# Performance work log

Hardware: AMD Instinct MI355X
Metric: run time of the kernel (lower is better)

Reference implementation:

```python
import jax, jax.numpy as jnp
import numpy as np


def setup_inputs() -> dict:
    key = jax.random.key(0)
    k1, k2 = jax.random.split(key)
    latents = jax.random.normal(k1, (32, 1024, 64), dtype=jnp.float32)
    codebook = jax.random.normal(k2, (8192, 64), dtype=jnp.float32)
    return {"latents": latents, "codebook": codebook}


def reference(latents, codebook):
    # Faithful to: cdist(latents_flat, codebook) -> argmin(dim=1) -> reshape(B, L)
    B, L, D = latents.shape
    x = latents.reshape(-1, D)                         # (N, D)
    x2 = jnp.sum(x * x, axis=1, keepdims=True)         # (N, 1)
    c2 = jnp.sum(codebook * codebook, axis=1)          # (K,)
    # (N, K) distance matrix, then argmin reduction
    d2 = x2 - 2.0 * (x @ codebook.T) + c2[None, :]
    indices = jnp.argmin(d2, axis=1)                   # (N,)
    return indices.reshape(B, L)
```

## Files before the change

### kernel.cpp

```cpp
#include <hip/hip_runtime.h>
#include <stdint.h>


#define N_TOTAL 32768
#define K_CODES 8192
#define EPS_GAP 0.008f

typedef __attribute__((ext_vector_type(4)))  float  floatx4;
typedef __attribute__((ext_vector_type(8)))  __bf16 bf16x8;

#define O_C2    0u
#define O_CBSW  32768u
#define O_PS1   2129920u
#define O_PS2   2654208u
#define O_PI1   3178496u
#define O_CNT   3702784u
#define O_LIST  3703040u
#define O_SLOT  3834112u
#define WS_NEED 4096256u

__device__ __forceinline__ unsigned int fkey(float s) {
    unsigned int u = __float_as_uint(s);
    return (u & 0x80000000u) ? ~u : (u | 0x80000000u);
}

__device__ __forceinline__ void load_lds16(const void* g, void* l) {
    __builtin_amdgcn_global_load_lds(
        (const __attribute__((address_space(1))) unsigned int*)g,
        (__attribute__((address_space(3))) unsigned int*)l, 16, 0, 0);
}

__global__ __launch_bounds__(256) void vq_prep(
    const float4* __restrict__ cb, uint4* __restrict__ cbSw,
    float* __restrict__ c2, int* __restrict__ cnt) {
    __shared__ float red[256];
    const int m = threadIdx.x & 31, g = threadIdx.x >> 5;
    const int rb = blockIdx.x;
    if (rb == 0 && threadIdx.x == 0) *cnt = 0;
    float4 a = cb[(size_t)(rb * 32 + m) * 16 + g * 2];
    float4 b = cb[(size_t)(rb * 32 + m) * 16 + g * 2 + 1];
    float x[8] = {a.x, a.y, a.z, a.w, b.x, b.y, b.z, b.w};
    bf16x8 hv, lv;
    float ss = 0.f;
#pragma unroll
    for (int i = 0; i < 8; ++i) {
        float v  = x[i];
        __bf16 hb = (__bf16)v;
        float r  = v - (float)hb;
        hv[i] = hb;
        lv[i] = (__bf16)r;
        ss += v * v;
    }
    cbSw[(size_t)rb * 512 + g * 32 + m]       = __builtin_bit_cast(uint4, hv);
    cbSw[(size_t)rb * 512 + (8 + g) * 32 + m] = __builtin_bit_cast(uint4, lv);
    red[threadIdx.x] = ss;
    __syncthreads();
    if (threadIdx.x < 32) {
        float s = 0.f;
#pragma unroll
        for (int gg = 0; gg < 8; ++gg) s += red[threadIdx.x + 32 * gg];
        c2[rb * 32 + threadIdx.x] = s;
    }
}

__global__ __launch_bounds__(256, 4) void vq_mfma(
    const float4* __restrict__ lat, const uint4* __restrict__ cbSw,
    const float* __restrict__ c2,
    float* __restrict__ pS1, float* __restrict__ pS2, int* __restrict__ pI1) {
    __shared__ uint4 Bs[2][1024];
    const int tid = threadIdx.x;
    const int wr = tid >> 6, lane = tid & 63;
    const int c16 = lane & 15, h4 = lane >> 4;

    const int q = blockIdx.x * 64 + wr * 16 + c16;
    bf16x8 aH[2], aL[2];
#pragma unroll
    for (int c = 0; c < 2; ++c) {
        float4 v0 = lat[(size_t)q * 16 + c * 8 + h4 * 2];
        float4 v1 = lat[(size_t)q * 16 + c * 8 + h4 * 2 + 1];
        float x[8] = {v0.x, v0.y, v0.z, v0.w, v1.x, v1.y, v1.z, v1.w};
#pragma unroll
        for (int j = 0; j < 8; ++j) {
            float v  = x[j];
            __bf16 hb = (__bf16)v;
            aH[c][j] = hb;
            aL[c][j] = (__bf16)(v - (float)hb);
        }
    }

    float t1[4], t2[4]; int i1[4];
#pragma unroll
    for (int r = 0; r < 4; ++r) { t1[r] = -3e38f; t2[r] = -3e38f; i1[r] = 0; }

    const int kBase = blockIdx.y * 2048;
    const uint4* srcBase = cbSw + ((size_t)(kBase >> 5) << 9);
    const float* c2g = c2 + kBase + c16;

    float ccCur[4], ccNxt[4];
#pragma unroll
    for (int T = 0; T < 4; ++T) ccCur[T] = c2g[T * 16];
#pragma unroll
    for (int i = 0; i < 4; ++i)
        load_lds16(&srcBase[wr * 256 + i * 64 + lane], &Bs[0][wr * 256 + i * 64]);
    __syncthreads();

    int cur = 0;
    for (int stage = 0; stage < 32; ++stage) {
        if (stage + 1 < 32) {
            const uint4* sp = srcBase + (size_t)(stage + 1) * 1024;
#pragma unroll
            for (int i = 0; i < 4; ++i)
                load_lds16(&sp[wr * 256 + i * 64 + lane],
                           &Bs[cur ^ 1][wr * 256 + i * 64]);
#pragma unroll
            for (int T = 0; T < 4; ++T)
                ccNxt[T] = c2g[(stage + 1) * 64 + T * 16];
        }

        const int colBase = kBase + stage * 64 + c16;

        __builtin_amdgcn_s_setprio(1);
#pragma unroll
        for (int T = 0; T < 4; ++T) {
            const float nn = -0.5f * ccCur[T];
            const int col = colBase + T * 16;
            const int bb = (T >> 1) * 512 + (T & 1) * 16 + c16 + h4 * 32;
            bf16x8 bH0 = __builtin_bit_cast(bf16x8, Bs[cur][bb]);
            bf16x8 bH1 = __builtin_bit_cast(bf16x8, Bs[cur][bb + 128]);
            bf16x8 bL0 = __builtin_bit_cast(bf16x8, Bs[cur][bb + 256]);
            bf16x8 bL1 = __builtin_bit_cast(bf16x8, Bs[cur][bb + 384]);
            floatx4 acc = {nn, nn, nn, nn};
            acc = __builtin_amdgcn_mfma_f32_16x16x32_bf16(aH[0], bH0, acc, 0, 0, 0);
            acc = __builtin_amdgcn_mfma_f32_16x16x32_bf16(aH[1], bH1, acc, 0, 0, 0);
            acc = __builtin_amdgcn_mfma_f32_16x16x32_bf16(aL[0], bH0, acc, 0, 0, 0);
            acc = __builtin_amdgcn_mfma_f32_16x16x32_bf16(aL[1], bH1, acc, 0, 0, 0);
            acc = __builtin_amdgcn_mfma_f32_16x16x32_bf16(aH[0], bL0, acc, 0, 0, 0);
            acc = __builtin_amdgcn_mfma_f32_16x16x32_bf16(aH[1], bL1, acc, 0, 0, 0);
#pragma unroll
            for (int r = 0; r < 4; ++r) {
                float a = acc[r];
                bool gt = a > t1[r];
                t2[r] = __builtin_amdgcn_fmed3f(a, t1[r], t2[r]);
                t1[r] = fmaxf(t1[r], a);
                i1[r] = gt ? col : i1[r];
            }
        }
        __builtin_amdgcn_s_setprio(0);

        __syncthreads();
#pragma unroll
        for (int T = 0; T < 4; ++T) ccCur[T] = ccNxt[T];
        cur ^= 1;
    }

#pragma unroll
    for (int mask = 1; mask <= 8; mask <<= 1) {
#pragma unroll
        for (int r = 0; r < 4; ++r) {
            float o1 = __shfl_xor(t1[r], mask);
            float o2 = __shfl_xor(t2[r], mask);
            int   oi = __shfl_xor(i1[r], mask);
            float n2 = fmaxf(fmaxf(t2[r], o2), fminf(t1[r], o1));
            bool take = (o1 > t1[r]) || (o1 == t1[r] && oi < i1[r]);
            t1[r] = take ? o1 : t1[r];
            i1[r] = take ? oi : i1[r];
            t2[r] = n2;
        }
    }

    if (c16 == 0) {
        const int o0 = blockIdx.y * N_TOTAL;
        const int qb = blockIdx.x * 64 + wr * 16 + h4 * 4;
#pragma unroll
        for (int r = 0; r < 4; ++r) {
            pS1[o0 + qb + r] = -2.f * t1[r];
            pS2[o0 + qb + r] = -2.f * t2[r];
            pI1[o0 + qb + r] = i1[r];
        }
    }
}

__global__ void vq_merge4(const float* __restrict__ pS1, const float* __restrict__ pS2,
                          const int* __restrict__ pI1, int* __restrict__ out,
                          int* __restrict__ cnt, int* __restrict__ list,
                          unsigned long long* __restrict__ slot) {
    int q = blockIdx.x * 256 + threadIdx.x;
    float g1 = 3e38f, g2 = 3e38f;
    int   gi = 0x7FFFFFFF;
#pragma unroll
    for (int p = 0; p < 4; ++p) {
        float s1p = pS1[p * N_TOTAL + q];
        float s2p = pS2[p * N_TOTAL + q];
        int   i1p = pI1[p * N_TOTAL + q];
        bool take = (s1p < g1) || (s1p == g1 && i1p < gi);
        g2 = fminf(g2, fminf(s2p, take ? g1 : s1p));
        if (take) { g1 = s1p; gi = i1p; }
    }
    out[q] = gi;
    if (g2 - g1 < EPS_GAP) {
        int e = atomicAdd(cnt, 1);
        list[e] = q;
        slot[e] = 0xFFFFFFFFFFFFFFFFull;
    }
}

__global__ __launch_bounds__(256) void vq_exact2(
    const float4* __restrict__ lat, const float4* __restrict__ cb,
    const float* __restrict__ c2, const int* __restrict__ cnt,
    const int* __restrict__ list, unsigned long long* __restrict__ slot) {
    __shared__ float qv[4][64];
    const int n = *cnt;
    const int totalChunks = n * 8;
    const int wInB = threadIdx.x >> 6;
    const int lane = threadIdx.x & 63;

    for (int base = blockIdx.x * 4; base < totalChunks; base += gridDim.x * 4) {
        const int c = base + wInB;
        const bool act = c < totalChunks;
        int e = 0, q = 0, kb = 0;
        if (act) { e = c >> 3; q = list[e]; kb = (c & 7) << 10; }
        __syncthreads();
        if (act && lane < 16) {
            float4 v = lat[(size_t)q * 16 + lane];
            *(float4*)&qv[wInB][lane * 4] = v;
        }
        __syncthreads();
        if (act) {
            float best = 3e38f; int bi = 0;
#pragma unroll 2
            for (int i = 0; i < 16; ++i) {
                const int k = kb + i * 64 + lane;
                float dot = 0.f;
#pragma unroll
                for (int d4 = 0; d4 < 16; ++d4) {
                    float4 cv = cb[(size_t)k * 16 + d4];
                    dot += qv[wInB][d4 * 4 + 0] * cv.x + qv[wInB][d4 * 4 + 1] * cv.y
                         + qv[wInB][d4 * 4 + 2] * cv.z + qv[wInB][d4 * 4 + 3] * cv.w;
                }
                float s = c2[k] - 2.f * dot;
                if (s < best) { best = s; bi = k; }
            }
            unsigned long long p = ((unsigned long long)fkey(best) << 32) | (unsigned)bi;
#pragma unroll
            for (int mask = 1; mask <= 32; mask <<= 1) {
                unsigned long long o = __shfl_xor(p, mask);
                p = o < p ? o : p;
            }
            if (lane == 0) atomicMin(&slot[e], p);
        }
    }
}

__global__ void vq_write(const int* __restrict__ cnt, const int* __restrict__ list,
                         const unsigned long long* __restrict__ slot,
                         int* __restrict__ out) {
    int t = blockIdx.x * 256 + threadIdx.x;
    if (t < *cnt) out[list[t]] = (int)(slot[t] & 0xFFFFFFFFull);
}

#define BM 128
#define BN 128
#define PAD 68

__global__ void vq_norms_fb(const float4* __restrict__ cb, float* __restrict__ c2) {
    int t = blockIdx.x * 256 + threadIdx.x;
    int r = t >> 2, p = t & 3;
    float s = 0.f;
#pragma unroll
    for (int i = 0; i < 4; ++i) {
        float4 v = cb[r * 16 + p * 4 + i];
        s += v.x * v.x + v.y * v.y + v.z * v.z + v.w * v.w;
    }
    s += __shfl_xor(s, 1);
    s += __shfl_xor(s, 2);
    if (p == 0) c2[r] = s;
}

__global__ __launch_bounds__(256) void vq_fp32(
    const float4* __restrict__ lat, const float4* __restrict__ cb,
    const float* __restrict__ c2, int ktPer,
    int* __restrict__ outIdx, float* __restrict__ partS, int* __restrict__ partI,
    int writePartial) {
    __shared__ float As[BM][PAD];
    __shared__ float Bsf[BN][PAD];
    __shared__ float c2s[BN];
    const int tid = threadIdx.x;
    const int tx = tid & 15;
    const int ty = tid >> 4;
    const int nBase = blockIdx.x * BM;
    const int kt0 = blockIdx.y * ktPer;
    const int ktN = kt0 + ktPer;
#pragma unroll
    for (int r = 0; r < 8; ++r) {
        int f = tid + 256 * r;
        int mm = f >> 4, d4 = f & 15;
        float4 v = lat[(size_t)(nBase + mm) * 16 + d4];
        *(float4*)&As[mm][d4 * 4] = v;
    }
    float best[8]; int bidx[8];
#pragma unroll
    for (int ii = 0; ii < 8; ++ii) { best[ii] = 3e38f; bidx[ii] = 0; }
    for (int kt = kt0; kt < ktN; ++kt) {
        const int kbase = kt * BN;
        __syncthreads();
#pragma unroll
        for (int r = 0; r < 8; ++r) {
            int f = tid + 256 * r;
            int k = f >> 4, d4 = f & 15;
            float4 v = cb[(size_t)(kbase + k) * 16 + d4];
            *(float4*)&Bsf[k][d4 * 4] = v;
        }
        if (tid < BN) c2s[tid] = c2[kbase + tid];
        __syncthreads();
        float acc[8][8];
#pragma unroll
        for (int ii = 0; ii < 8; ++ii)
#pragma unroll
            for (int jj = 0; jj < 8; ++jj) acc[ii][jj] = 0.f;
#pragma unroll 4
        for (int d4 = 0; d4 < 16; ++d4) {
            float4 a[8], b[8];
#pragma unroll
            for (int ii = 0; ii < 8; ++ii) a[ii] = *(const float4*)&As[tx + 16 * ii][d4 * 4];
#pragma unroll
            for (int jj = 0; jj < 8; ++jj) b[jj] = *(const float4*)&Bsf[ty + 16 * jj][d4 * 4];
#pragma unroll
            for (int ii = 0; ii < 8; ++ii)
#pragma unroll
                for (int jj = 0; jj < 8; ++jj)
                    acc[ii][jj] += a[ii].x * b[jj].x + a[ii].y * b[jj].y
                                 + a[ii].z * b[jj].z + a[ii].w * b[jj].w;
        }
#pragma unroll
        for (int jj = 0; jj < 8; ++jj) {
            int k = kbase + ty + 16 * jj;
            float cc = c2s[ty + 16 * jj];
#pragma unroll
            for (int ii = 0; ii < 8; ++ii) {
                float s = cc - 2.f * acc[ii][jj];
                if (s < best[ii]) { best[ii] = s; bidx[ii] = k; }
            }
        }
    }
    __syncthreads();
    float* redS = &As[0][0];
    int*   redI = (int*)&Bsf[0][0];
#pragma unroll
    for (int ii = 0; ii < 8; ++ii) {
        int mm = tx + 16 * ii;
        redS[ty * BM + mm] = best[ii];
        redI[ty * BM + mm] = bidx[ii];
    }
    __syncthreads();
    if (tid < BM) {
        int mm = tid;
        float bs = redS[mm]; int bi = redI[mm];
#pragma unroll
        for (int t = 1; t < 16; ++t) {
            float s = redS[t * BM + mm]; int i = redI[t * BM + mm];
            if (s < bs || (s == bs && i < bi)) { bs = s; bi = i; }
        }
        int n = nBase + mm;
        if (writePartial) { partS[blockIdx.y * N_TOTAL + n] = bs; partI[blockIdx.y * N_TOTAL + n] = bi; }
        else outIdx[n] = bi;
    }
}

__global__ void vq_merge_fb(const float* __restrict__ partS, const int* __restrict__ partI,
                            int* __restrict__ out) {
    int n = blockIdx.x * 256 + threadIdx.x;
    float s0 = partS[n], s1 = partS[N_TOTAL + n];
    int   i0 = partI[n], i1 = partI[N_TOTAL + n];
    out[n] = (s1 < s0) ? i1 : i0;
}

extern "C" void kernel_launch(void* const* d_in, const int* in_sizes, int n_in,
                              void* d_out, int out_size, void* d_ws, size_t ws_size,
                              hipStream_t stream) {
    const float4* lat = (const float4*)d_in[0];
    const float4* cb  = (const float4*)d_in[1];
    int* out = (int*)d_out;
    char* ws = (char*)d_ws;

    if (ws_size >= WS_NEED) {
        float* c2   = (float*)(ws + O_C2);
        uint4* cbSw = (uint4*)(ws + O_CBSW);
        float* pS1  = (float*)(ws + O_PS1);
        float* pS2  = (float*)(ws + O_PS2);
        int*   pI1  = (int*)(ws + O_PI1);
        int*   cnt  = (int*)(ws + O_CNT);
        int*   list = (int*)(ws + O_LIST);
        unsigned long long* slot = (unsigned long long*)(ws + O_SLOT);

        vq_prep<<<256, 256, 0, stream>>>(cb, cbSw, c2, cnt);
        vq_mfma<<<dim3(512, 4), 256, 0, stream>>>(lat, cbSw, c2, pS1, pS2, pI1);
        vq_merge4<<<128, 256, 0, stream>>>(pS1, pS2, pI1, out, cnt, list, slot);
        vq_exact2<<<1024, 256, 0, stream>>>(lat, cb, c2, cnt, list, slot);
        vq_write<<<128, 256, 0, stream>>>(cnt, list, slot, out);
    } else {
        float* c2 = (float*)ws;
        vq_norms_fb<<<128, 256, 0, stream>>>(cb, c2);
        const size_t needSplit = 32768u + 2u * N_TOTAL * 4u + 2u * N_TOTAL * 4u + 64u;
        if (ws_size >= needSplit) {
            float* partS = (float*)(ws + 32768);
            int*   partI = (int*)(ws + 32768 + 2 * N_TOTAL * 4);
            dim3 grid(N_TOTAL / BM, 2);
            vq_fp32<<<grid, 256, 0, stream>>>(lat, cb, c2, (K_CODES / BN) / 2, out, partS, partI, 1);
            vq_merge_fb<<<N_TOTAL / 256, 256, 0, stream>>>(partS, partI, out);
        } else {
            dim3 grid(N_TOTAL / BM, 1);
            vq_fp32<<<grid, 256, 0, stream>>>(lat, cb, c2, K_CODES / BN, out, nullptr, nullptr, 0);
        }
    }
}
```

Baseline: 214.3 us.

## Process two query tiles per wave to reuse codebook fragments

Each wave now computes two 16-row query tiles against every loaded codebook fragment, doubling the queries per block to 128 and halving the grid. This halves LDS reads and global codebook staging per query and amortizes the c2 loads. In exchange, register pressure rises from doubled A fragments and top-2 state, and fewer blocks are available for latency hiding.

```diff
diff --git a/kernel.cpp b/kernel.cpp
--- a/kernel.cpp
+++ b/kernel.cpp
@@ -72,25 +72,29 @@
     const int wr = tid >> 6, lane = tid & 63;
     const int c16 = lane & 15, h4 = lane >> 4;
 
-    const int q = blockIdx.x * 64 + wr * 16 + c16;
-    bf16x8 aH[2], aL[2];
+    const int q0 = blockIdx.x * 128 + wr * 32 + c16;
+    bf16x8 aH[2][2], aL[2][2];
+#pragma unroll
+    for (int qt = 0; qt < 2; ++qt)
 #pragma unroll
     for (int c = 0; c < 2; ++c) {
-        float4 v0 = lat[(size_t)q * 16 + c * 8 + h4 * 2];
-        float4 v1 = lat[(size_t)q * 16 + c * 8 + h4 * 2 + 1];
+        float4 v0 = lat[(size_t)(q0 + qt * 16) * 16 + c * 8 + h4 * 2];
+        float4 v1 = lat[(size_t)(q0 + qt * 16) * 16 + c * 8 + h4 * 2 + 1];
         float x[8] = {v0.x, v0.y, v0.z, v0.w, v1.x, v1.y, v1.z, v1.w};
 #pragma unroll
         for (int j = 0; j < 8; ++j) {
             float v  = x[j];
             __bf16 hb = (__bf16)v;
-            aH[c][j] = hb;
-            aL[c][j] = (__bf16)(v - (float)hb);
-        }
-    }
-
-    float t1[4], t2[4]; int i1[4];
-#pragma unroll
-    for (int r = 0; r < 4; ++r) { t1[r] = -3e38f; t2[r] = -3e38f; i1[r] = 0; }
+            aH[qt][c][j] = hb;
+            aL[qt][c][j] = (__bf16)(v - (float)hb);
+        }
+    }
+
+    float t1[2][4], t2[2][4]; int i1[2][4];
+#pragma unroll
+    for (int qt = 0; qt < 2; ++qt)
+#pragma unroll
+    for (int r = 0; r < 4; ++r) { t1[qt][r] = -3e38f; t2[qt][r] = -3e38f; i1[qt][r] = 0; }
 
     const int kBase = blockIdx.y * 2048;
     const uint4* srcBase = cbSw + ((size_t)(kBase >> 5) << 9);
@@ -129,20 +133,23 @@
             bf16x8 bH1 = __builtin_bit_cast(bf16x8, Bs[cur][bb + 128]);
             bf16x8 bL0 = __builtin_bit_cast(bf16x8, Bs[cur][bb + 256]);
             bf16x8 bL1 = __builtin_bit_cast(bf16x8, Bs[cur][bb + 384]);
-            floatx4 acc = {nn, nn, nn, nn};
-            acc = __builtin_amdgcn_mfma_f32_16x16x32_bf16(aH[0], bH0, acc, 0, 0, 0);
-            acc = __builtin_amdgcn_mfma_f32_16x16x32_bf16(aH[1], bH1, acc, 0, 0, 0);
-            acc = __builtin_amdgcn_mfma_f32_16x16x32_bf16(aL[0], bH0, acc, 0, 0, 0);
-            acc = __builtin_amdgcn_mfma_f32_16x16x32_bf16(aL[1], bH1, acc, 0, 0, 0);
-            acc = __builtin_amdgcn_mfma_f32_16x16x32_bf16(aH[0], bL0, acc, 0, 0, 0);
-            acc = __builtin_amdgcn_mfma_f32_16x16x32_bf16(aH[1], bL1, acc, 0, 0, 0);
-#pragma unroll
-            for (int r = 0; r < 4; ++r) {
-                float a = acc[r];
-                bool gt = a > t1[r];
-                t2[r] = __builtin_amdgcn_fmed3f(a, t1[r], t2[r]);
-                t1[r] = fmaxf(t1[r], a);
-                i1[r] = gt ? col : i1[r];
+#pragma unroll
+            for (int qt = 0; qt < 2; ++qt) {
+                floatx4 acc = {nn, nn, nn, nn};
+                acc = __builtin_amdgcn_mfma_f32_16x16x32_bf16(aH[qt][0], bH0, acc, 0, 0, 0);
+                acc = __builtin_amdgcn_mfma_f32_16x16x32_bf16(aH[qt][1], bH1, acc, 0, 0, 0);
+                acc = __builtin_amdgcn_mfma_f32_16x16x32_bf16(aL[qt][0], bH0, acc, 0, 0, 0);
+                acc = __builtin_amdgcn_mfma_f32_16x16x32_bf16(aL[qt][1], bH1, acc, 0, 0, 0);
+                acc = __builtin_amdgcn_mfma_f32_16x16x32_bf16(aH[qt][0], bL0, acc, 0, 0, 0);
+                acc = __builtin_amdgcn_mfma_f32_16x16x32_bf16(aH[qt][1], bL1, acc, 0, 0, 0);
+#pragma unroll
+                for (int r = 0; r < 4; ++r) {
+                    float a = acc[r];
+                    bool gt = a > t1[qt][r];
+                    t2[qt][r] = __builtin_amdgcn_fmed3f(a, t1[qt][r], t2[qt][r]);
+                    t1[qt][r] = fmaxf(t1[qt][r], a);
+                    i1[qt][r] = gt ? col : i1[qt][r];
+                }
             }
         }
         __builtin_amdgcn_s_setprio(0);
@@ -156,26 +163,31 @@
 #pragma unroll
     for (int mask = 1; mask <= 8; mask <<= 1) {
 #pragma unroll
+        for (int qt = 0; qt < 2; ++qt)
+#pragma unroll
         for (int r = 0; r < 4; ++r) {
-            float o1 = __shfl_xor(t1[r], mask);
-            float o2 = __shfl_xor(t2[r], mask);
-            int   oi = __shfl_xor(i1[r], mask);
-            float n2 = fmaxf(fmaxf(t2[r], o2), fminf(t1[r], o1));
-            bool take = (o1 > t1[r]) || (o1 == t1[r] && oi < i1[r]);
-            t1[r] = take ? o1 : t1[r];
-            i1[r] = take ? oi : i1[r];
-            t2[r] = n2;
+            float o1 = __shfl_xor(t1[qt][r], mask);
+            float o2 = __shfl_xor(t2[qt][r], mask);
+            int   oi = __shfl_xor(i1[qt][r], mask);
+            float n2 = fmaxf(fmaxf(t2[qt][r], o2), fminf(t1[qt][r], o1));
+            bool take = (o1 > t1[qt][r]) || (o1 == t1[qt][r] && oi < i1[qt][r]);
+            t1[qt][r] = take ? o1 : t1[qt][r];
+            i1[qt][r] = take ? oi : i1[qt][r];
+            t2[qt][r] = n2;
         }
     }
 
     if (c16 == 0) {
         const int o0 = blockIdx.y * N_TOTAL;
-        const int qb = blockIdx.x * 64 + wr * 16 + h4 * 4;
-#pragma unroll
-        for (int r = 0; r < 4; ++r) {
-            pS1[o0 + qb + r] = -2.f * t1[r];
-            pS2[o0 + qb + r] = -2.f * t2[r];
-            pI1[o0 + qb + r] = i1[r];
+#pragma unroll
+        for (int qt = 0; qt < 2; ++qt) {
+            const int qb = blockIdx.x * 128 + wr * 32 + qt * 16 + h4 * 4;
+#pragma unroll
+            for (int r = 0; r < 4; ++r) {
+                pS1[o0 + qb + r] = -2.f * t1[qt][r];
+                pS2[o0 + qb + r] = -2.f * t2[qt][r];
+                pI1[o0 + qb + r] = i1[qt][r];
+            }
         }
     }
 }
@@ -393,7 +405,7 @@
         unsigned long long* slot = (unsigned long long*)(ws + O_SLOT);
 
         vq_prep<<<256, 256, 0, stream>>>(cb, cbSw, c2, cnt);
-        vq_mfma<<<dim3(512, 4), 256, 0, stream>>>(lat, cbSw, c2, pS1, pS2, pI1);
+        vq_mfma<<<dim3(256, 4), 256, 0, stream>>>(lat, cbSw, c2, pS1, pS2, pI1);
         vq_merge4<<<128, 256, 0, stream>>>(pS1, pS2, pI1, out, cnt, list, slot);
         vq_exact2<<<1024, 256, 0, stream>>>(lat, cb, c2, cnt, list, slot);
         vq_write<<<128, 256, 0, stream>>>(cnt, list, slot, out);
```

Result: faster. 193.2 us (-9.8%).
